# Performance work log

Hardware: AMD Instinct MI355X
Metric: run time of the kernel (lower is better)

Reference implementation:

```python
import jax, jax.numpy as jnp
import numpy as np

NEG = -9e15
EPS = 1e-5

# GraphAttention (classic GAT layer): h = xW; e_ij = LeakyReLU(a1.h_i + a2.h_j);
# attention = softmax(where(adj>0, e, -9e15)); out = attention @ h.
# The torch code builds one big block-diagonal adjacency; off-block entries get
# -9e15 and underflow to exactly 0 after softmax, so batched per-block GAT is
# numerically identical and avoids the O((B*N)^2) dense waste.

def gat(x, adj, W, a1, a2):
    h = jnp.einsum('bnf,fh->bnh', x, W)
    e = jax.nn.leaky_relu(jnp.einsum('bnh,h->bn', h, a1)[:, :, None]
                          + jnp.einsum('bnh,h->bn', h, a2)[:, None, :], 0.2)
    att = jax.nn.softmax(jnp.where(adj > 0, e, NEG), axis=-1)
    return jnp.einsum('bnm,bmh->bnh', att, h)

def mlp(x, W1, b1, W2, b2):
    return jax.nn.relu(x @ W1 + b1) @ W2 + b2


def setup_inputs() -> dict:
    key = jax.random.key(0)
    ks = iter(jax.random.split(key, 40))
    B, NV, NO = 8, 500, 1500
    DV, DO, H = 512, 32, 128

    def mat(din, dout):
        return jax.random.normal(next(ks), (din, dout), jnp.float32) / np.sqrt(din)

    def vec(d):
        return jax.random.normal(next(ks), (d,), jnp.float32) * 0.1

    inp = {
        'vis_memory': jax.random.normal(next(ks), (B, NV, DV), jnp.float32),
        'obj_memory': jax.random.normal(next(ks), (B, NO, DO), jnp.float32),
        'vis_adj': jax.random.uniform(next(ks), (B, NV, NV), jnp.float32),
        'obj_adj': jax.random.uniform(next(ks), (B, NO, NO), jnp.float32),
        'object_A_OV': jax.random.uniform(next(ks), (B, NO, NV), jnp.float32),
        # GAT layers
        'Wv1': mat(DV, H), 'av1a': vec(H), 'av1b': vec(H),
        'Wv2': mat(H, H),  'av2a': vec(H), 'av2b': vec(H),
        'Wo1': mat(DO, H), 'ao1a': vec(H), 'ao1b': vec(H),
        'Wo2': mat(H, H),  'ao2a': vec(H), 'ao2b': vec(H),
        # globalTobject / objectTglobal MLPs
        'g2o_W1': mat(H, H), 'g2o_b1': jnp.zeros((H,), jnp.float32),
        'g2o_W2': mat(H, H), 'g2o_b2': jnp.zeros((H,), jnp.float32),
        'o2g_W1': mat(H, H), 'o2g_b1': jnp.zeros((H,), jnp.float32),
        'o2g_W2': mat(H, H), 'o2g_b2': jnp.zeros((H,), jnp.float32),
        # output projections
        'img_W': mat(H, DV), 'img_b': jnp.zeros((DV,), jnp.float32),
        'obj_W': mat(H, DO), 'obj_b': jnp.zeros((DO,), jnp.float32),
    }
    return inp


def reference(vis_memory, obj_memory, vis_adj, obj_adj, object_A_OV,
              Wv1, av1a, av1b, Wv2, av2a, av2b,
              Wo1, ao1a, ao1b, Wo2, ao2a, ao2b,
              g2o_W1, g2o_b1, g2o_W2, g2o_b2,
              o2g_W1, o2g_b1, o2g_W2, o2g_b2,
              img_W, img_b, obj_W, obj_b):
    # cross adjacencies (block-diagonal in torch -> batched here)
    vo = jnp.swapaxes(object_A_OV, 1, 2)            # (B, NV, NO)
    vo = vo / (vo.sum(2, keepdims=True) + EPS)
    ov = jnp.swapaxes(vo, 1, 2)                     # (B, NO, NV)
    ov = ov / (ov.sum(2, keepdims=True) + EPS)

    v1 = jax.nn.relu(gat(vis_memory, vis_adj, Wv1, av1a, av1b))
    o1 = jax.nn.relu(gat(obj_memory, obj_adj, Wo1, ao1a, ao1b))
    vis = v1 + mlp(jnp.einsum('bvo,boh->bvh', vo, o1), o2g_W1, o2g_b1, o2g_W2, o2g_b2)
    obj = o1 + mlp(jnp.einsum('bov,bvh->boh', ov, v1), g2o_W1, g2o_b1, g2o_W2, g2o_b2)

    v2 = jax.nn.relu(gat(vis, vis_adj, Wv2, av2a, av2b))
    o2 = jax.nn.relu(gat(obj, obj_adj, Wo2, ao2a, ao2b))
    vis = v2 + mlp(jnp.einsum('bvo,boh->bvh', vo, o2), o2g_W1, o2g_b1, o2g_W2, o2g_b2)
    obj = o2 + mlp(jnp.einsum('bov,bvh->boh', ov, v2), g2o_W1, g2o_b1, g2o_W2, g2o_b2)

    vis_out = vis @ img_W + img_b                   # (B, NV, DV)
    obj_out = obj @ obj_W + obj_b                   # (B, NO, DO)
    return (vis_out, obj_out)
```

## Files before the change

### kernel.cpp

```cpp
#include <hip/hip_runtime.h>
#include <math.h>

#define EPSV 1e-5f
#define HD 128
#define IT 64
#define JT 32
#define WP 68
#define CCH 16
#define THR 256

typedef __attribute__((address_space(3))) uint32_t lds_u32_t;
typedef __attribute__((address_space(1))) uint32_t gbl_u32_t;
typedef __attribute__((ext_vector_type(8))) short bf16x8;
typedef __attribute__((ext_vector_type(4))) float f32x4;

__device__ __forceinline__ void async_copy16(const float* g, float* l) {
    __builtin_amdgcn_global_load_lds((const gbl_u32_t*)g, (lds_u32_t*)l, 16, 0, 0);
}

__device__ __forceinline__ void stage_tile_async(const float* gsrc, float* lds, int t) {
    int wv = t >> 6, lane = t & 63;
#pragma unroll
    for (int it = 0; it < 4; ++it) {
        int c = it * 4 + wv;
        async_copy16(gsrc + c * 256 + lane * 4, lds + c * 256);
    }
}

__device__ __forceinline__ void stage_8k(const void* g, void* l, int t) {
    const float* gf = (const float*)g; float* lf = (float*)l;
    async_copy16(gf + t * 4, lf + t * 4);
    async_copy16(gf + t * 4 + 1024, lf + t * 4 + 1024);
}

__device__ __forceinline__ unsigned int f2bf(float f) {
    return __builtin_bit_cast(unsigned int, f) >> 16;
}

__device__ __forceinline__ unsigned short rne_bf16(float f) {
    unsigned int u = __builtin_bit_cast(unsigned int, f);
    u += 0x7FFFu + ((u >> 16) & 1u);
    return (unsigned short)(u >> 16);
}

struct WprepP { const float *W, *a1, *a2; unsigned short* WT; float *wa1, *wa2; int K; };
struct XprepP { const float* X; unsigned short* Xbf; const float *wa1, *wa2;
                float *sa, *sb; int rows; };
struct GmfP   { const unsigned short *Xbf, *WT; unsigned short* hT; int N, tilesJ; };
struct AggP  { const float *adj, *sa, *sb, *sm; const unsigned short* hT;
               float *pp, *zp; int N, tiles, tilesJ, tps; };
struct CrossP{ const float *A, *src, *rs1; float *pp; int iN, jN, tiles, tps; };
struct FinP  { const float *pp, *zp; float *out; int rows, S; };
struct MlpP  { const float *pp, *scale; int S; const float *W1, *b1, *W2, *b2, *res;
               float *out; int rows; };


__global__ void colsum_part_k(const float* __restrict__ A, float* __restrict__ s1p,
                              int B, int NO, int NV) {
    int v = blockIdx.x * 256 + threadIdx.x;
    int c = blockIdx.y, b = blockIdx.z;
    if (v >= NV) return;
    int chunk = (NO + CCH - 1) / CCH;
    int o0 = c * chunk;
    int o1 = o0 + chunk; if (o1 > NO) o1 = NO;
    const float* Ab = A + (size_t)b * NO * NV + v;
    float s = 0.f;
    for (int o = o0; o < o1; ++o) s += Ab[(size_t)o * NV];
    s1p[((size_t)b * CCH + c) * NV + v] = s;
}

__global__ void colsum_fin_k(const float* __restrict__ s1p, float* __restrict__ rs1,
                             int B, int NV) {
    int idx = blockIdx.x * 256 + threadIdx.x;
    if (idx >= B * NV) return;
    int b = idx / NV, v = idx - b * NV;
    float s = 0.f;
    for (int c = 0; c < CCH; ++c) s += s1p[((size_t)b * CCH + c) * NV + v];
    rs1[idx] = 1.f / (s + EPSV);
}

__global__ void rowsum_inv_k(const float* __restrict__ A, const float* __restrict__ rs1,
                             float* __restrict__ rs2, int B, int NO, int NV) {
    int row = blockIdx.x * (blockDim.x >> 6) + (threadIdx.x >> 6);
    int lane = threadIdx.x & 63;
    if (row >= B * NO) return;
    int b = row / NO;
    const float* Ar = A + (size_t)row * NV;
    const float* r1 = rs1 + (size_t)b * NV;
    float s = 0.f;
    for (int v = lane; v < NV; v += 64) s += Ar[v] * r1[v];
    for (int off = 32; off; off >>= 1) s += __shfl_xor(s, off, 64);
    if (lane == 0) rs2[row] = 1.f / (s + EPSV);
}

__global__ __launch_bounds__(256)
void wprep_k(WprepP p0, WprepP p1, WprepP p2, WprepP p3, int e0, int e1, int e2) {
    __shared__ float lw[32][129];
    __shared__ float a1s[128], a2s[128];
    int bid = blockIdx.x;
    const WprepP& P = bid < e0 ? p0 : bid < e1 ? p1 : bid < e2 ? p2 : p3;
    int lb = bid < e0 ? bid : bid < e1 ? bid - e0 : bid < e2 ? bid - e1 : bid - e2;
    int k0 = lb * 32, K = P.K;
    int t = threadIdx.x;
    if (t < 128) { a1s[t] = P.a1[t]; a2s[t] = P.a2[t]; }
    for (int idx = t; idx < 32 * 32; idx += 256) {
        int kk = idx >> 5, c4 = idx & 31;
        float4 v = ((const float4*)(P.W + (size_t)(k0 + kk) * 128))[c4];
        lw[kk][c4 * 4 + 0] = v.x; lw[kk][c4 * 4 + 1] = v.y;
        lw[kk][c4 * 4 + 2] = v.z; lw[kk][c4 * 4 + 3] = v.w;
    }
    __syncthreads();
    int kk = t >> 3, g = t & 7;
    float s1 = 0.f, s2 = 0.f;
    for (int c = g; c < 128; c += 8) {
        float w = lw[kk][c];
        s1 = fmaf(w, a1s[c], s1);
        s2 = fmaf(w, a2s[c], s2);
    }
    s1 += __shfl_xor(s1, 1, 64); s1 += __shfl_xor(s1, 2, 64); s1 += __shfl_xor(s1, 4, 64);
    s2 += __shfl_xor(s2, 1, 64); s2 += __shfl_xor(s2, 2, 64); s2 += __shfl_xor(s2, 4, 64);
    if (g == 0) { P.wa1[k0 + kk] = s1; P.wa2[k0 + kk] = s2; }
    for (int idx = t; idx < 4096; idx += 256) {
        int c = idx >> 5, k = idx & 31;
        P.WT[(size_t)c * K + k0 + k] = rne_bf16(lw[k][c]);
    }
}

template<int K>
__device__ void xprep_body(const XprepP& P, int lb) {
    int t = threadIdx.x, wv = t >> 6, lane = t & 63;
    int row = lb * 4 + wv;
    if (row >= P.rows) return;
    const float4* x4 = (const float4*)(P.X + (size_t)row * K);
    const float4* w14 = (const float4*)P.wa1;
    const float4* w24 = (const float4*)P.wa2;
    unsigned short* xb = P.Xbf + (size_t)row * K;
    float s1 = 0.f, s2 = 0.f;
    constexpr int K4 = K / 4;
    constexpr int NI = (K4 + 63) / 64;
#pragma unroll
    for (int i = 0; i < NI; ++i) {
        int k4 = i * 64 + lane;
        if ((K4 % 64 == 0) || (k4 < K4)) {
            float4 x = x4[k4];
            float4 a = w14[k4];
            float4 b = w24[k4];
            s1 += x.x * a.x + x.y * a.y + x.z * a.z + x.w * a.w;
            s2 += x.x * b.x + x.y * b.y + x.z * b.z + x.w * b.w;
            ushort4 p = make_ushort4(rne_bf16(x.x), rne_bf16(x.y),
                                     rne_bf16(x.z), rne_bf16(x.w));
            *(ushort4*)(xb + (size_t)k4 * 4) = p;
        }
    }
#pragma unroll
    for (int off = 32; off; off >>= 1) {
        s1 += __shfl_xor(s1, off, 64);
        s2 += __shfl_xor(s2, off, 64);
    }
    if (lane == 0) { P.sa[row] = s1; P.sb[row] = s2; }
}

template<int KV, int KO>
__global__ __launch_bounds__(256)
void xprep2_k(XprepP V, XprepP O, int GV) {
    int bid = blockIdx.x;
    if (bid < GV) xprep_body<KV>(V, bid);
    else          xprep_body<KO>(O, bid - GV);
}

template<int K>
__device__ void gmf_body(const GmfP& P, int lb) {
    int tilesJ = P.tilesJ, N = P.N;
    int b = lb / tilesJ, jt = lb - b * tilesJ;
    int t = threadIdx.x, wv = t >> 6, lane = t & 63;
    int ml = lane & 15, quad = lane >> 4;
    const unsigned short* xb = P.Xbf + ((size_t)b * N + (size_t)jt * 32) * K;
    const unsigned short* wt0 = P.WT + (size_t)(wv * 32 + ml) * K;
    const unsigned short* wt1 = wt0 + (size_t)16 * K;
    const unsigned short* xb0 = xb + (size_t)ml * K;
    const unsigned short* xb1 = xb + (size_t)(16 + ml) * K;
    f32x4 acc00 = {0.f, 0.f, 0.f, 0.f}, acc01 = acc00, acc10 = acc00, acc11 = acc00;
#pragma unroll 4
    for (int kt = 0; kt < K / 32; ++kt) {
        int kk = kt * 32 + quad * 8;
        bf16x8 a0 = *(const bf16x8*)(wt0 + kk);
        bf16x8 a1 = *(const bf16x8*)(wt1 + kk);
        bf16x8 b0 = *(const bf16x8*)(xb0 + kk);
        bf16x8 b1 = *(const bf16x8*)(xb1 + kk);
        acc00 = __builtin_amdgcn_mfma_f32_16x16x32_bf16(a0, b0, acc00, 0, 0, 0);
        acc01 = __builtin_amdgcn_mfma_f32_16x16x32_bf16(a0, b1, acc01, 0, 0, 0);
        acc10 = __builtin_amdgcn_mfma_f32_16x16x32_bf16(a1, b0, acc10, 0, 0, 0);
        acc11 = __builtin_amdgcn_mfma_f32_16x16x32_bf16(a1, b1, acc11, 0, 0, 0);
    }
    unsigned short* hb = P.hT + (size_t)(b * tilesJ + jt) * 4096;
    int nvalid = N - jt * 32; if (nvalid > 32) nvalid = 32;
    bool ok0 = ml < nvalid, ok1 = (16 + ml) < nvalid;
    int c0 = wv * 32 + quad * 4;
#pragma unroll
    for (int r = 0; r < 4; ++r) {
        hb[(size_t)(c0 + r) * 32 + ml]           = ok0 ? rne_bf16(acc00[r]) : 0;
        hb[(size_t)(c0 + r) * 32 + 16 + ml]      = ok1 ? rne_bf16(acc01[r]) : 0;
        hb[(size_t)(c0 + 16 + r) * 32 + ml]      = ok0 ? rne_bf16(acc10[r]) : 0;
        hb[(size_t)(c0 + 16 + r) * 32 + 16 + ml] = ok1 ? rne_bf16(acc11[r]) : 0;
    }
}

template<int KV, int KO>
__global__ __launch_bounds__(256)
void gmf2_k(GmfP V, GmfP O, int GV) {
    int bid = blockIdx.x;
    if (bid < GV) gmf_body<KV>(V, bid);
    else          gmf_body<KO>(O, bid - GV);
}

__global__ __launch_bounds__(256)
void sbmax2_k(const float* __restrict__ sbV, float* __restrict__ smV,
              const float* __restrict__ sbO, float* __restrict__ smO,
              int NV, int NO) {
    __shared__ float red[256];
    int b0 = blockIdx.x, t = threadIdx.x;
    const float* sb; float* out; int N;
    if (b0 < 8) { sb = sbV + (size_t)b0 * NV; out = smV + b0; N = NV; }
    else        { sb = sbO + (size_t)(b0 - 8) * NO; out = smO + (b0 - 8); N = NO; }
    float m = -INFINITY;
    for (int j = t; j < N; j += 256) m = fmaxf(m, sb[j]);
    red[t] = m; __syncthreads();
    for (int s = 128; s; s >>= 1) {
        if (t < s) red[t] = fmaxf(red[t], red[t + s]);
        __syncthreads();
    }
    if (t == 0) *out = red[0];
}

struct SharedAggM {
    unsigned short hsT[2][128][32];
    unsigned short wsA[2][4][64][8];
    float sa_s[IT], m_s[IT];
};

__device__ void agg_body(SharedAggM& sm, const AggP& P, int lbid) {
    int tiles = P.tiles;
    int split = lbid / (8 * tiles);
    int rem = lbid - split * 8 * tiles;
    int b = rem / tiles;
    int i0 = (rem - b * tiles) * IT;
    int N = P.N;
    int jt0 = split * P.tps;
    if (jt0 >= P.tilesJ) return;
    int jt1 = jt0 + P.tps; if (jt1 > P.tilesJ) jt1 = P.tilesJ;
    int T = jt1 - jt0;
    int t = threadIdx.x;
    if (t < IT) {
        int i = i0 + t;
        float s = (i < N) ? P.sa[(size_t)b * N + i] : 0.f;
        sm.sa_s[t] = s;
        float e = s + P.sm[b];
        sm.m_s[t] = e > 0.f ? e : 0.2f * e;
    }
    __syncthreads();
    int wv = t >> 6, lane = t & 63;
    int il = t >> 2, j4 = (t & 3) * 4;
    int q0 = j4 >> 3, i0w = j4 & 7, wrow = il & 15;
    int nquad = lane >> 4, nlow = lane & 15;
    f32x4 acc[8];
#pragma unroll
    for (int nt = 0; nt < 8; ++nt)
#pragma unroll
        for (int r = 0; r < 4; ++r) acc[nt][r] = 0.f;
    float zacc = 0.f;
    const float* adjb = P.adj + ((size_t)b * N + i0) * N;
    const float* sbb = P.sb + (size_t)b * N;
    const unsigned short* hTb = P.hT + ((size_t)b * P.tilesJ + jt0) * 4096;
    int irow = i0 + il;
    stage_8k(hTb, &sm.hsT[0][0][0], t);
    float4 a4[2], s4[2];
#pragma unroll
    for (int k = 0; k < 2; ++k) {
        int j = jt0 * JT + j4 + k * 16;
        float4 av = make_float4(0.f,0.f,0.f,0.f), sv = make_float4(0.f,0.f,0.f,0.f);
        if (irow < N) {
            if (j + 3 < N) {
                av = *(const float4*)&adjb[(size_t)il * N + j];
                sv = *(const float4*)&sbb[j];
            } else {
                float* ap = (float*)&av; float* sp = (float*)&sv;
                for (int r = 0; r < 4; ++r)
                    if (j + r < N) { ap[r] = adjb[(size_t)il * N + j + r]; sp[r] = sbb[j + r]; }
            }
        }
        a4[k] = av; s4[k] = sv;
    }
    for (int tt = 0; tt < T; ++tt) {
        int cur = tt & 1;
        float sai = sm.sa_s[il], m = sm.m_s[il];
#pragma unroll
        for (int k = 0; k < 2; ++k) {
            float av[4] = {a4[k].x, a4[k].y, a4[k].z, a4[k].w};
            float sv[4] = {s4[k].x, s4[k].y, s4[k].z, s4[k].w};
            float w[4];
#pragma unroll
            for (int r = 0; r < 4; ++r) {
                float e = sai + sv[r];
                e = e > 0.f ? e : 0.2f * e;
                w[r] = av[r] > 0.f ? __expf(e - m) : 0.f;
                zacc += w[r];
            }
            unsigned int lo = f2bf(w[0]) | (__builtin_bit_cast(unsigned int, w[1]) & 0xFFFF0000u);
            unsigned int hi = f2bf(w[2]) | (__builtin_bit_cast(unsigned int, w[3]) & 0xFFFF0000u);
            uint2 pk = make_uint2(lo, hi);
            *(uint2*)&sm.wsA[cur][wv][wrow + 16 * (q0 + 2 * k)][i0w] = pk;
        }
        __syncthreads();
        if (tt + 1 < T) {
            stage_8k(hTb + (size_t)(tt + 1) * 4096, &sm.hsT[1 - cur][0][0], t);
#pragma unroll
            for (int k = 0; k < 2; ++k) {
                int j = (jt0 + tt + 1) * JT + j4 + k * 16;
                float4 av = make_float4(0.f,0.f,0.f,0.f), sv = make_float4(0.f,0.f,0.f,0.f);
                if (irow < N) {
                    if (j + 3 < N) {
                        av = *(const float4*)&adjb[(size_t)il * N + j];
                        sv = *(const float4*)&sbb[j];
                    } else {
                        float* ap = (float*)&av; float* sp = (float*)&sv;
                        for (int r = 0; r < 4; ++r)
                            if (j + r < N) { ap[r] = adjb[(size_t)il * N + j + r]; sp[r] = sbb[j + r]; }
                    }
                }
                a4[k] = av; s4[k] = sv;
            }
        }
        bf16x8 afrag = *(const bf16x8*)&sm.wsA[cur][wv][lane][0];
#pragma unroll
        for (int nt = 0; nt < 8; ++nt) {
            bf16x8 bfrag = *(const bf16x8*)&sm.hsT[cur][nt * 16 + nlow][nquad * 8];
            acc[nt] = __builtin_amdgcn_mfma_f32_16x16x32_bf16(afrag, bfrag, acc[nt], 0, 0, 0);
        }
    }
    zacc += __shfl_xor(zacc, 1, 64);
    zacc += __shfl_xor(zacc, 2, 64);
    size_t rowsTot = (size_t)8 * N;
    float* pp = P.pp + ((size_t)split * rowsTot + (size_t)b * N) * HD;
#pragma unroll
    for (int nt = 0; nt < 8; ++nt)
#pragma unroll
        for (int r = 0; r < 4; ++r) {
            int row = i0 + wv * 16 + nquad * 4 + r;
            if (row < N) pp[(size_t)row * HD + nt * 16 + nlow] = acc[nt][r];
        }
    if ((t & 3) == 0 && irow < N)
        P.zp[(size_t)split * rowsTot + (size_t)b * N + irow] = zacc;
}

__global__ __launch_bounds__(256)
void agg2_k(AggP V, AggP O, int GVb) {
    __shared__ SharedAggM sm;
    int bid = blockIdx.x;
    if (bid < GVb) agg_body(sm, V, bid);
    else           agg_body(sm, O, bid - GVb);
}

__device__ __forceinline__ void tile_fma256(const float (*hs)[HD], const float (*ws)[WP],
                                            int rg, int c0, float acc[4][8]) {
#pragma unroll 8
    for (int jl = 0; jl < JT; ++jl) {
        float4 h0 = *(const float4*)&hs[jl][c0];
        float4 h1 = *(const float4*)&hs[jl][c0 + 64];
        float4 w4 = *(const float4*)&ws[jl][rg * 4];
        float wq[4] = {w4.x, w4.y, w4.z, w4.w};
#pragma unroll
        for (int q = 0; q < 4; ++q) {
            float w = wq[q];
            acc[q][0] = fmaf(w, h0.x, acc[q][0]);
            acc[q][1] = fmaf(w, h0.y, acc[q][1]);
            acc[q][2] = fmaf(w, h0.z, acc[q][2]);
            acc[q][3] = fmaf(w, h0.w, acc[q][3]);
            acc[q][4] = fmaf(w, h1.x, acc[q][4]);
            acc[q][5] = fmaf(w, h1.y, acc[q][5]);
            acc[q][6] = fmaf(w, h1.z, acc[q][6]);
            acc[q][7] = fmaf(w, h1.w, acc[q][7]);
        }
    }
}

__device__ __forceinline__ void part_store256(float* __restrict__ pp, size_t base,
                                              int i0, int N, int rg, int c0,
                                              float acc[4][8]) {
#pragma unroll
    for (int q = 0; q < 4; ++q) {
        int i = i0 + rg * 4 + q;
        if (i >= N) continue;
        float* op = pp + base + (size_t)i * HD;
        *(float4*)&op[c0]      = make_float4(acc[q][0], acc[q][1], acc[q][2], acc[q][3]);
        *(float4*)&op[c0 + 64] = make_float4(acc[q][4], acc[q][5], acc[q][6], acc[q][7]);
    }
}

struct SharedTile { float hs[2][JT][HD]; float ws[2][JT][WP]; };

__device__ void cross_vo_body(SharedTile& sm, const CrossP& P, int lbid) {
    int tiles = P.tiles;
    int split = lbid / (8 * tiles);
    int rem = lbid - split * 8 * tiles;
    int b = rem / tiles;
    int i0 = (rem - b * tiles) * IT;
    int NVl = P.iN, NOl = P.jN;
    int j_begin = split * P.tps * JT;
    if (j_begin >= NOl) return;
    int j_end = j_begin + P.tps * JT;
    if (j_end > NOl) j_end = NOl;
    int T = (j_end - j_begin + JT - 1) / JT;
    int t = threadIdx.x;
    int rg = t >> 4, c0 = (t & 15) * 4;
    int il = t & 63, jlb = t >> 6;
    float acc[4][8];
#pragma unroll
    for (int q = 0; q < 4; ++q)
#pragma unroll
        for (int x = 0; x < 8; ++x) acc[q][x] = 0.f;
    const float* Ab = P.A + (size_t)b * NOl * NVl;
    const float* srcb = P.src + (size_t)b * NOl * HD;
    int v = i0 + il;
    float w8[8];
    stage_tile_async(srcb + (size_t)j_begin * HD, &sm.hs[0][0][0], t);
#pragma unroll
    for (int k = 0; k < 8; ++k) {
        int o = j_begin + jlb + k * 4;
        w8[k] = (v < NVl && o < NOl) ? Ab[(size_t)o * NVl + v] : 0.f;
    }
    for (int tt = 0; tt < T; ++tt) {
        int cur = tt & 1;
#pragma unroll
        for (int k = 0; k < 8; ++k) sm.ws[cur][jlb + k * 4][il] = w8[k];
        __syncthreads();
        if (tt + 1 < T) {
            int jn = j_begin + (tt + 1) * JT;
            stage_tile_async(srcb + (size_t)jn * HD, &sm.hs[1 - cur][0][0], t);
#pragma unroll
            for (int k = 0; k < 8; ++k) {
                int o = jn + jlb + k * 4;
                w8[k] = (v < NVl && o < NOl) ? Ab[(size_t)o * NVl + v] : 0.f;
            }
        }
        tile_fma256(sm.hs[cur], sm.ws[cur], rg, c0, acc);
    }
    size_t rowsTot = (size_t)8 * NVl;
    part_store256(P.pp, ((size_t)split * rowsTot + (size_t)b * NVl) * HD, i0, NVl, rg, c0, acc);
}

__device__ void cross_ov_body(SharedTile& sm, const CrossP& P, int lbid) {
    int tiles = P.tiles;
    int split = lbid / (8 * tiles);
    int rem = lbid - split * 8 * tiles;
    int b = rem / tiles;
    int i0 = (rem - b * tiles) * IT;
    int NOl = P.iN, NVl = P.jN;
    int j_begin = split * P.tps * JT;
    if (j_begin >= NVl) return;
    int j_end = j_begin + P.tps * JT;
    if (j_end > NVl) j_end = NVl;
    int T = (j_end - j_begin + JT - 1) / JT;
    int t = threadIdx.x;
    int rg = t >> 4, c0 = (t & 15) * 4;
    int il = t >> 2, j4 = (t & 3) * 4;
    float acc[4][8];
#pragma unroll
    for (int q = 0; q < 4; ++q)
#pragma unroll
        for (int x = 0; x < 8; ++x) acc[q][x] = 0.f;
    const float* Ab = P.A + (size_t)b * NOl * NVl;
    const float* srcb = P.src + (size_t)b * NVl * HD;
    const float* r1b = P.rs1 + (size_t)b * NVl;
    int orow = i0 + il;
    float4 a4[2], r4[2];
    stage_tile_async(srcb + (size_t)j_begin * HD, &sm.hs[0][0][0], t);
#pragma unroll
    for (int k = 0; k < 2; ++k) {
        int vv = j_begin + j4 + k * 16;
        float4 av = make_float4(0.f,0.f,0.f,0.f), rv = make_float4(0.f,0.f,0.f,0.f);
        if (orow < NOl) {
            if (vv + 3 < NVl) {
                av = *(const float4*)&Ab[(size_t)orow * NVl + vv];
                rv = *(const float4*)&r1b[vv];
            } else {
                float* ap = (float*)&av; float* rp = (float*)&rv;
                for (int r = 0; r < 4; ++r)
                    if (vv + r < NVl) { ap[r] = Ab[(size_t)orow * NVl + vv + r]; rp[r] = r1b[vv + r]; }
            }
        }
        a4[k] = av; r4[k] = rv;
    }
    for (int tt = 0; tt < T; ++tt) {
        int cur = tt & 1;
#pragma unroll
        for (int k = 0; k < 2; ++k) {
            float wv[4] = {a4[k].x * r4[k].x, a4[k].y * r4[k].y,
                           a4[k].z * r4[k].z, a4[k].w * r4[k].w};
#pragma unroll
            for (int r = 0; r < 4; ++r) sm.ws[cur][j4 + r + k * 16][il] = wv[r];
        }
        __syncthreads();
        if (tt + 1 < T) {
            int jn = j_begin + (tt + 1) * JT;
            stage_tile_async(srcb + (size_t)jn * HD, &sm.hs[1 - cur][0][0], t);
#pragma unroll
            for (int k = 0; k < 2; ++k) {
                int vv = jn + j4 + k * 16;
                float4 av = make_float4(0.f,0.f,0.f,0.f), rv = make_float4(0.f,0.f,0.f,0.f);
                if (orow < NOl) {
                    if (vv + 3 < NVl) {
                        av = *(const float4*)&Ab[(size_t)orow * NVl + vv];
                        rv = *(const float4*)&r1b[vv];
                    } else {
                        float* ap = (float*)&av; float* rp = (float*)&rv;
                        for (int r = 0; r < 4; ++r)
                            if (vv + r < NVl) { ap[r] = Ab[(size_t)orow * NVl + vv + r]; rp[r] = r1b[vv + r]; }
                    }
                }
                a4[k] = av; r4[k] = rv;
            }
        }
        tile_fma256(sm.hs[cur], sm.ws[cur], rg, c0, acc);
    }
    size_t rowsTot = (size_t)8 * NOl;
    part_store256(P.pp, ((size_t)split * rowsTot + (size_t)b * NOl) * HD, i0, NOl, rg, c0, acc);
}

__global__ __launch_bounds__(256)
void cross2_k(CrossP VO, CrossP OV, int GVOb) {
    __shared__ SharedTile sm;
    int bid = blockIdx.x;
    if (bid < GVOb) cross_vo_body(sm, VO, bid);
    else            cross_ov_body(sm, OV, bid - GVOb);
}

__global__ __launch_bounds__(256)
void fin2_k(FinP V, FinP O, int GVb) {
    int bid = blockIdx.x;
    const FinP& P = (bid < GVb) ? V : O;
    int idx = ((bid < GVb) ? bid : bid - GVb) * 256 + threadIdx.x;
    int rows = P.rows;
    int row = idx >> 5;
    if (row >= rows) return;
    float4 v = make_float4(0.f, 0.f, 0.f, 0.f);
    for (int s = 0; s < P.S; ++s) {
        float4 p = ((const float4*)P.pp)[((size_t)s * rows + row) * 32 + (idx & 31)];
        v.x += p.x; v.y += p.y; v.z += p.z; v.w += p.w;
    }
    float z = 0.f;
    for (int s = 0; s < P.S; ++s) z += P.zp[(size_t)s * rows + row];
    float sc = 1.f / z;
    v.x = fmaxf(v.x * sc, 0.f); v.y = fmaxf(v.y * sc, 0.f);
    v.z = fmaxf(v.z * sc, 0.f); v.w = fmaxf(v.w * sc, 0.f);
    ((float4*)P.out)[idx] = v;
}

__global__ __launch_bounds__(128)
void mlp2_k(MlpP V, MlpP O, int GVb) {
    __shared__ float xs[8][HD];
    __shared__ float hh[8][HD];
    int bid = blockIdx.x;
    const MlpP& P = (bid < GVb) ? V : O;
    int row0 = ((bid < GVb) ? bid : bid - GVb) * 8;
    int rows = P.rows;
    int t = threadIdx.x;
    for (int l = t; l < 8 * 32; l += 128) {
        int r = l >> 5, c4 = l & 31;
        int row = row0 + r;
        float4 v = make_float4(0.f, 0.f, 0.f, 0.f);
        if (row < rows) {
            for (int s = 0; s < P.S; ++s) {
                float4 p = ((const float4*)P.pp)[((size_t)s * rows + row) * 32 + c4];
                v.x += p.x; v.y += p.y; v.z += p.z; v.w += p.w;
            }
            float sc = P.scale[row];
            v.x *= sc; v.y *= sc; v.z *= sc; v.w *= sc;
        }
        ((float4*)&xs[r][0])[c4] = v;
    }
    __syncthreads();
    int wv = t >> 6, tt = t & 63, rb = wv * 4;
    float a0[4] = {0.f, 0.f, 0.f, 0.f}, a1v[4] = {0.f, 0.f, 0.f, 0.f};
#pragma unroll 4
    for (int k = 0; k < HD; ++k) {
        float w0 = P.W1[(size_t)k * HD + tt];
        float w1 = P.W1[(size_t)k * HD + tt + 64];
#pragma unroll
        for (int r = 0; r < 4; ++r) {
            float x = xs[rb + r][k];
            a0[r] = fmaf(x, w0, a0[r]);
            a1v[r] = fmaf(x, w1, a1v[r]);
        }
    }
    float bb0 = P.b1[tt], bb1 = P.b1[tt + 64];
#pragma unroll
    for (int r = 0; r < 4; ++r) {
        hh[rb + r][tt]      = fmaxf(a0[r] + bb0, 0.f);
        hh[rb + r][tt + 64] = fmaxf(a1v[r] + bb1, 0.f);
    }
    __syncthreads();
    float c0a[4] = {0.f, 0.f, 0.f, 0.f}, c1a[4] = {0.f, 0.f, 0.f, 0.f};
#pragma unroll 4
    for (int k = 0; k < HD; ++k) {
        float w0 = P.W2[(size_t)k * HD + tt];
        float w1 = P.W2[(size_t)k * HD + tt + 64];
#pragma unroll
        for (int r = 0; r < 4; ++r) {
            float x = hh[rb + r][k];
            c0a[r] = fmaf(x, w0, c0a[r]);
            c1a[r] = fmaf(x, w1, c1a[r]);
        }
    }
    float d0 = P.b2[tt], d1 = P.b2[tt + 64];
#pragma unroll
    for (int r = 0; r < 4; ++r) {
        int row = row0 + rb + r;
        if (row >= rows) continue;
        P.out[(size_t)row * HD + tt]      = c0a[r] + d0 + P.res[(size_t)row * HD + tt];
        P.out[(size_t)row * HD + tt + 64] = c1a[r] + d1 + P.res[(size_t)row * HD + tt + 64];
    }
}

template<int RELU, int BIAS, int RES>
__global__ __launch_bounds__(128)
void linear_k(const float* __restrict__ X, const float* __restrict__ W,
              const float* __restrict__ bias, const float* __restrict__ res,
              float* __restrict__ out, int rows, int K, int Dout) {
    __shared__ float xs[4][512];
    int row0 = blockIdx.x * 4;
    int t = threadIdx.x;
    int K4 = K >> 2;
    for (int l = t; l < 4 * K4; l += 128) {
        int r = l / K4, c4 = l - r * K4;
        float4 val = make_float4(0.f, 0.f, 0.f, 0.f);
        if (row0 + r < rows) val = ((const float4*)(X + (size_t)(row0 + r) * K))[c4];
        ((float4*)&xs[r][0])[c4] = val;
    }
    __syncthreads();
    int chunk = Dout < 256 ? Dout : 256;
    int half = chunk >> 1;
    if (t >= half) return;
    int c0 = blockIdx.y * chunk + t;
    int c1 = c0 + half;
    float a00 = 0, a01 = 0, a02 = 0, a03 = 0, a10 = 0, a11 = 0, a12 = 0, a13 = 0;
#pragma unroll 4
    for (int k = 0; k < K; ++k) {
        float w0 = W[(size_t)k * Dout + c0];
        float w1 = W[(size_t)k * Dout + c1];
        float x0 = xs[0][k], x1 = xs[1][k], x2 = xs[2][k], x3 = xs[3][k];
        a00 = fmaf(x0, w0, a00); a01 = fmaf(x1, w0, a01);
        a02 = fmaf(x2, w0, a02); a03 = fmaf(x3, w0, a03);
        a10 = fmaf(x0, w1, a10); a11 = fmaf(x1, w1, a11);
        a12 = fmaf(x2, w1, a12); a13 = fmaf(x3, w1, a13);
    }
    float accs[2][4] = {{a00, a01, a02, a03}, {a10, a11, a12, a13}};
    int cs[2] = {c0, c1};
    for (int h = 0; h < 2; ++h) {
        float bv = BIAS ? bias[cs[h]] : 0.f;
        for (int r = 0; r < 4; ++r) {
            int row = row0 + r;
            if (row >= rows) continue;
            float v = accs[h][r] + bv;
            if (RES) v += res[(size_t)row * Dout + cs[h]];
            if (RELU) v = fmaxf(v, 0.f);
            out[(size_t)row * Dout + cs[h]] = v;
        }
    }
}

extern "C" void kernel_launch(void* const* d_in, const int* in_sizes, int n_in,
                              void* d_out, int out_size, void* d_ws, size_t ws_size,
                              hipStream_t stream) {
    const int B = 8, NV = 500, NO = 1500, DV = 512, DO = 32;
    const float* vis_memory = (const float*)d_in[0];
    const float* obj_memory = (const float*)d_in[1];
    const float* vis_adj    = (const float*)d_in[2];
    const float* obj_adj    = (const float*)d_in[3];
    const float* A_OV       = (const float*)d_in[4];
    const float* Wv1  = (const float*)d_in[5];
    const float* av1a = (const float*)d_in[6];
    const float* av1b = (const float*)d_in[7];
    const float* Wv2  = (const float*)d_in[8];
    const float* av2a = (const float*)d_in[9];
    const float* av2b = (const float*)d_in[10];
    const float* Wo1  = (const float*)d_in[11];
    const float* ao1a = (const float*)d_in[12];
    const float* ao1b = (const float*)d_in[13];
    const float* Wo2  = (const float*)d_in[14];
    const float* ao2a = (const float*)d_in[15];
    const float* ao2b = (const float*)d_in[16];
    const float* g2o_W1 = (const float*)d_in[17];
    const float* g2o_b1 = (const float*)d_in[18];
    const float* g2o_W2 = (const float*)d_in[19];
    const float* g2o_b2 = (const float*)d_in[20];
    const float* o2g_W1 = (const float*)d_in[21];
    const float* o2g_b1 = (const float*)d_in[22];
    const float* o2g_W2 = (const float*)d_in[23];
    const float* o2g_b2 = (const float*)d_in[24];
    const float* img_W = (const float*)d_in[25];
    const float* img_b = (const float*)d_in[26];
    const float* obj_W = (const float*)d_in[27];
    const float* obj_b = (const float*)d_in[28];

    const int tilesJV = 16, tilesJO = 47;

    float* wsp = (float*)d_ws;
    size_t off = 0;
    auto alloc = [&](size_t n) { float* p = wsp + off; off += (n + 3) & ~(size_t)3; return p; };
    float* rs1   = alloc(B * NV);
    float* rs2   = alloc(B * NO);
    float* saV   = alloc(B * NV);
    float* sbV   = alloc(B * NV);
    float* smV   = alloc(B);
    float* saO   = alloc(B * NO);
    float* sbO   = alloc(B * NO);
    float* smO   = alloc(B);
    float* s1p   = alloc((size_t)B * CCH * NV);
    unsigned short* WTv1 = (unsigned short*)alloc(128 * 512 / 2);
    unsigned short* WTo1 = (unsigned short*)alloc(128 * 32 / 2);
    unsigned short* WTv2 = (unsigned short*)alloc(128 * 128 / 2);
    unsigned short* WTo2 = (unsigned short*)alloc(128 * 128 / 2);
    float* wav1a = alloc(512); float* wav1b = alloc(512);
    float* wao1a = alloc(32);  float* wao1b = alloc(32);
    float* wav2a = alloc(128); float* wav2b = alloc(128);
    float* wao2a = alloc(128); float* wao2b = alloc(128);
    unsigned short* XbfV = (unsigned short*)alloc((size_t)B * NV * 512 / 2);
    unsigned short* XbfO = (unsigned short*)alloc((size_t)B * NO * 128 / 2);
    unsigned short* hTv = (unsigned short*)alloc((size_t)B * tilesJV * 4096 / 2);
    unsigned short* hTo = (unsigned short*)alloc((size_t)B * tilesJO * 4096 / 2);
    float* v1    = alloc((size_t)B * NV * HD);
    float* o1    = alloc((size_t)B * NO * HD);
    float* visb  = alloc((size_t)B * NV * HD);
    float* objb  = alloc((size_t)B * NO * HD);
    float* ppV   = alloc((size_t)8 * B * NV * HD);
    float* zpV   = alloc((size_t)8 * B * NV);
    float* ppO   = alloc((size_t)4 * B * NO * HD);
    float* zpO   = alloc((size_t)4 * B * NO);
    alloc(16384);

    {
        WprepP w0{Wv1, av1a, av1b, WTv1, wav1a, wav1b, DV};
        WprepP w1{Wo1, ao1a, ao1b, WTo1, wao1a, wao1b, DO};
        WprepP w2{Wv2, av2a, av2b, WTv2, wav2a, wav2b, HD};
        WprepP w3{Wo2, ao2a, ao2b, WTo2, wao2a, wao2b, HD};
        wprep_k<<<25, 256, 0, stream>>>(w0, w1, w2, w3, 16, 17, 21);
    }

    colsum_part_k<<<dim3((NV + 255) / 256, CCH, B), 256, 0, stream>>>(A_OV, s1p, B, NO, NV);
    colsum_fin_k<<<dim3((B * NV + 255) / 256), 256, 0, stream>>>(s1p, rs1, B, NV);
    rowsum_inv_k<<<dim3((B * NO + 3) / 4), 256, 0, stream>>>(A_OV, rs1, rs2, B, NO, NV);

    const int tilesV = 8, tilesO = 24;
    const int SV = 8, SO = 4, SVO = 8, SOV = 4;
    const int tpsV = 2;
    const int tpsO = 12;
    const int tpsVO = 6;
    const int tpsOV = 4;
    const int G_AGG_V = B * tilesV * SV;
    const int G_AGG_O = B * tilesO * SO;
    const int G_CR_VO = B * tilesV * SVO;
    const int G_CR_OV = B * tilesO * SOV;
    const int G_MLP_V = B * NV / 8;
    const int G_MLP_O = B * NO / 8;
    const int G_FIN_V = B * NV * 32 / 256;
    const int G_FIN_O = B * NO * 32 / 256;
    const int G_XP_V = B * NV / 4;
    const int G_XP_O = B * NO / 4;
    const int G_GMF_V = B * tilesJV;
    const int G_GMF_O = B * tilesJO;

    auto tail = [&](float* visout, float* objout) {
        sbmax2_k<<<16, 256, 0, stream>>>(sbV, smV, sbO, smO, NV, NO);
        AggP av{vis_adj, saV, sbV, smV, hTv, ppV, zpV, NV, tilesV, tilesJV, tpsV};
        AggP ao{obj_adj, saO, sbO, smO, hTo, ppO, zpO, NO, tilesO, tilesJO, tpsO};
        agg2_k<<<G_AGG_V + G_AGG_O, THR, 0, stream>>>(av, ao, G_AGG_V);
        FinP fv{ppV, zpV, v1, B * NV, SV};
        FinP fo{ppO, zpO, o1, B * NO, SO};
        fin2_k<<<G_FIN_V + G_FIN_O, 256, 0, stream>>>(fv, fo, G_FIN_V);
        CrossP cvo{A_OV, o1, nullptr, ppV, NV, NO, tilesV, tpsVO};
        CrossP cov{A_OV, v1, rs1, ppO, NO, NV, tilesO, tpsOV};
        cross2_k<<<G_CR_VO + G_CR_OV, THR, 0, stream>>>(cvo, cov, G_CR_VO);
        MlpP mv{ppV, rs1, SVO, o2g_W1, o2g_b1, o2g_W2, o2g_b2, v1, visout, B * NV};
        MlpP mo{ppO, rs2, SOV, g2o_W1, g2o_b1, g2o_W2, g2o_b2, o1, objout, B * NO};
        mlp2_k<<<G_MLP_V + G_MLP_O, 128, 0, stream>>>(mv, mo, G_MLP_V);
    };

    {
        XprepP xv{vis_memory, XbfV, wav1a, wav1b, saV, sbV, B * NV};
        XprepP xo{obj_memory, XbfO, wao1a, wao1b, saO, sbO, B * NO};
        xprep2_k<512, 32><<<G_XP_V + G_XP_O, 256, 0, stream>>>(xv, xo, G_XP_V);
        GmfP gv{XbfV, WTv1, hTv, NV, tilesJV};
        GmfP go{XbfO, WTo1, hTo, NO, tilesJO};
        gmf2_k<512, 32><<<G_GMF_V + G_GMF_O, 256, 0, stream>>>(gv, go, G_GMF_V);
        tail(visb, objb);
    }
    {
        XprepP xv{visb, XbfV, wav2a, wav2b, saV, sbV, B * NV};
        XprepP xo{objb, XbfO, wao2a, wao2b, saO, sbO, B * NO};
        xprep2_k<128, 128><<<G_XP_V + G_XP_O, 256, 0, stream>>>(xv, xo, G_XP_V);
        GmfP gv{XbfV, WTv2, hTv, NV, tilesJV};
        GmfP go{XbfO, WTo2, hTo, NO, tilesJO};
        gmf2_k<128, 128><<<G_GMF_V + G_GMF_O, 256, 0, stream>>>(gv, go, G_GMF_V);
        tail(visb, objb);
    }

    float* vis_out = (float*)d_out;
    float* obj_out = vis_out + (size_t)B * NV * DV;
    linear_k<0, 1, 0><<<dim3((B * NV + 3) / 4, (DV + 255) / 256), 128, 0, stream>>>(
        visb, img_W, img_b, nullptr, vis_out, B * NV, HD, DV);
    linear_k<0, 1, 0><<<dim3((B * NO + 3) / 4, 1), 128, 0, stream>>>(
        objb, obj_W, obj_b, nullptr, obj_out, B * NO, HD, DO);
}
```

Before: 615.0 us.

## Deepen adjacency prefetch to two tiles with manual waitcnt and unrolled double buffer

```diff
diff --git a/kernel.cpp b/kernel.cpp
--- a/kernel.cpp
+++ b/kernel.cpp
@@ -238,6 +238,57 @@
     float sa_s[IT], m_s[IT];
 };
 
+__device__ __forceinline__ void load_adj(const float* adjb, const float* sbb,
+                                         int il, int j4, int irow, int N,
+                                         int jt, float4* AR, float4* SR) {
+#pragma unroll
+    for (int k = 0; k < 2; ++k) {
+        int j = jt * JT + j4 + k * 16;
+        bool okc = (j + 3) < N;
+        bool ok = (irow < N) && okc;
+        size_t offa = ok ? (size_t)il * N + j : 0;
+        int offs = okc ? j : 0;
+        float4 av = *(const float4*)(adjb + offa);
+        float4 sv = *(const float4*)(sbb + offs);
+        float msk = ok ? 1.f : 0.f;
+        av.x *= msk; av.y *= msk; av.z *= msk; av.w *= msk;
+        AR[k] = av; SR[k] = sv;
+    }
+}
+
+#define AGG_TILE(tt_, CUR_, AR_, SR_) do {                                          \
+    float sai_ = sm.sa_s[il], mm_ = sm.m_s[il];                                     \
+    _Pragma("unroll")                                                               \
+    for (int k = 0; k < 2; ++k) {                                                   \
+        float av_[4] = {AR_[k].x, AR_[k].y, AR_[k].z, AR_[k].w};                    \
+        float sv_[4] = {SR_[k].x, SR_[k].y, SR_[k].z, SR_[k].w};                    \
+        float w_[4];                                                                \
+        _Pragma("unroll")                                                           \
+        for (int r = 0; r < 4; ++r) {                                               \
+            float e_ = sai_ + sv_[r];                                               \
+            e_ = e_ > 0.f ? e_ : 0.2f * e_;                                         \
+            w_[r] = av_[r] > 0.f ? __expf(e_ - mm_) : 0.f;                          \
+            zacc += w_[r];                                                          \
+        }                                                                           \
+        unsigned int lo_ = f2bf(w_[0]) | (__builtin_bit_cast(unsigned int, w_[1]) & 0xFFFF0000u); \
+        unsigned int hi_ = f2bf(w_[2]) | (__builtin_bit_cast(unsigned int, w_[3]) & 0xFFFF0000u); \
+        *(uint2*)&sm.wsA[CUR_][wv][wrow + 16 * (q0 + 2 * k)][i0w] = make_uint2(lo_, hi_); \
+    }                                                                               \
+       \
+    if (tt_ + 1 < T) asm volatile("s_waitcnt vmcnt(4) lgkmcnt(0)" ::: "memory");    \
+    else             asm volatile("s_waitcnt vmcnt(0) lgkmcnt(0)" ::: "memory");    \
+    __builtin_amdgcn_s_barrier();                                                   \
+    asm volatile("" ::: "memory");      \
+    if (tt_ + 1 < T) stage_8k(hTb + (size_t)(tt_ + 1) * 4096, &sm.hsT[1 - CUR_][0][0], t); \
+    if (tt_ + 2 < T) load_adj(adjb, sbb, il, j4, irow, N, jt0 + tt_ + 2, AR_, SR_); \
+    bf16x8 afrag_ = *(const bf16x8*)&sm.wsA[CUR_][wv][lane][0];                     \
+    _Pragma("unroll")                                                               \
+    for (int nt = 0; nt < 8; ++nt) {                                                \
+        bf16x8 bfrag_ = *(const bf16x8*)&sm.hsT[CUR_][nt * 16 + nlow][nquad * 8];   \
+        acc[nt] = __builtin_amdgcn_mfma_f32_16x16x32_bf16(afrag_, bfrag_, acc[nt], 0, 0, 0); \
+    }                                                                               \
+} while (0)
+
 __device__ void agg_body(SharedAggM& sm, const AggP& P, int lbid) {
     int tiles = P.tiles;
     int split = lbid / (8 * tiles);
@@ -272,70 +323,16 @@
     const float* sbb = P.sb + (size_t)b * N;
     const unsigned short* hTb = P.hT + ((size_t)b * P.tilesJ + jt0) * 4096;
     int irow = i0 + il;
+    float4 aA[2], sA[2], aB[2], sB[2];
     stage_8k(hTb, &sm.hsT[0][0][0], t);
-    float4 a4[2], s4[2];
-#pragma unroll
-    for (int k = 0; k < 2; ++k) {
-        int j = jt0 * JT + j4 + k * 16;
-        float4 av = make_float4(0.f,0.f,0.f,0.f), sv = make_float4(0.f,0.f,0.f,0.f);
-        if (irow < N) {
-            if (j + 3 < N) {
-                av = *(const float4*)&adjb[(size_t)il * N + j];
-                sv = *(const float4*)&sbb[j];
-            } else {
-                float* ap = (float*)&av; float* sp = (float*)&sv;
-                for (int r = 0; r < 4; ++r)
-                    if (j + r < N) { ap[r] = adjb[(size_t)il * N + j + r]; sp[r] = sbb[j + r]; }
-            }
-        }
-        a4[k] = av; s4[k] = sv;
-    }
-    for (int tt = 0; tt < T; ++tt) {
-        int cur = tt & 1;
-        float sai = sm.sa_s[il], m = sm.m_s[il];
-#pragma unroll
-        for (int k = 0; k < 2; ++k) {
-            float av[4] = {a4[k].x, a4[k].y, a4[k].z, a4[k].w};
-            float sv[4] = {s4[k].x, s4[k].y, s4[k].z, s4[k].w};
-            float w[4];
-#pragma unroll
-            for (int r = 0; r < 4; ++r) {
-                float e = sai + sv[r];
-                e = e > 0.f ? e : 0.2f * e;
-                w[r] = av[r] > 0.f ? __expf(e - m) : 0.f;
-                zacc += w[r];
-            }
-            unsigned int lo = f2bf(w[0]) | (__builtin_bit_cast(unsigned int, w[1]) & 0xFFFF0000u);
-            unsigned int hi = f2bf(w[2]) | (__builtin_bit_cast(unsigned int, w[3]) & 0xFFFF0000u);
-            uint2 pk = make_uint2(lo, hi);
-            *(uint2*)&sm.wsA[cur][wv][wrow + 16 * (q0 + 2 * k)][i0w] = pk;
-        }
-        __syncthreads();
-        if (tt + 1 < T) {
-            stage_8k(hTb + (size_t)(tt + 1) * 4096, &sm.hsT[1 - cur][0][0], t);
-#pragma unroll
-            for (int k = 0; k < 2; ++k) {
-                int j = (jt0 + tt + 1) * JT + j4 + k * 16;
-                float4 av = make_float4(0.f,0.f,0.f,0.f), sv = make_float4(0.f,0.f,0.f,0.f);
-                if (irow < N) {
-                    if (j + 3 < N) {
-                        av = *(const float4*)&adjb[(size_t)il * N + j];
-                        sv = *(const float4*)&sbb[j];
-                    } else {
-                        float* ap = (float*)&av; float* sp = (float*)&sv;
-                        for (int r = 0; r < 4; ++r)
-                            if (j + r < N) { ap[r] = adjb[(size_t)il * N + j + r]; sp[r] = sbb[j + r]; }
-                    }
-                }
-                a4[k] = av; s4[k] = sv;
-            }
-        }
-        bf16x8 afrag = *(const bf16x8*)&sm.wsA[cur][wv][lane][0];
-#pragma unroll
-        for (int nt = 0; nt < 8; ++nt) {
-            bf16x8 bfrag = *(const bf16x8*)&sm.hsT[cur][nt * 16 + nlow][nquad * 8];
-            acc[nt] = __builtin_amdgcn_mfma_f32_16x16x32_bf16(afrag, bfrag, acc[nt], 0, 0, 0);
-        }
+    load_adj(adjb, sbb, il, j4, irow, N, jt0, aA, sA);
+    if (1 < T) load_adj(adjb, sbb, il, j4, irow, N, jt0 + 1, aB, sB);
+    int tt = 0;
+    while (true) {
+        AGG_TILE(tt, 0, aA, sA);
+        ++tt; if (tt >= T) break;
+        AGG_TILE(tt, 1, aB, sB);
+        ++tt; if (tt >= T) break;
     }
     zacc += __shfl_xor(zacc, 1, 64);
     zacc += __shfl_xor(zacc, 2, 64);
```

After: 601.2 us. 2.2% less time.

## Precompute adjacency bitmasks once, swizzle hT layout, triple-buffer agg staging

Applied to the files above, without the earlier changes.

```diff
diff --git a/kernel.cpp b/kernel.cpp
--- a/kernel.cpp
+++ b/kernel.cpp
@@ -47,7 +47,8 @@
 struct XprepP { const float* X; unsigned short* Xbf; const float *wa1, *wa2;
                 float *sa, *sb; int rows; };
 struct GmfP   { const unsigned short *Xbf, *WT; unsigned short* hT; int N, tilesJ; };
-struct AggP  { const float *adj, *sa, *sb, *sm; const unsigned short* hT;
+struct MaskP  { const float* adj; unsigned int* maskT; int N, tilesJ, chunks; };
+struct AggP  { const unsigned int* mask; const float *sa, *sb, *sm; const unsigned short* hT;
                float *pp, *zp; int N, tiles, tilesJ, tps; };
 struct CrossP{ const float *A, *src, *rs1; float *pp; int iN, jN, tiles, tps; };
 struct FinP  { const float *pp, *zp; float *out; int rows, S; };
@@ -91,6 +92,27 @@
     for (int v = lane; v < NV; v += 64) s += Ar[v] * r1[v];
     for (int off = 32; off; off >>= 1) s += __shfl_xor(s, off, 64);
     if (lane == 0) rs2[row] = 1.f / (s + EPSV);
+}
+
+__global__ __launch_bounds__(256)
+void mask2_k(MaskP V, MaskP O, int GV) {
+    int bid = blockIdx.x;
+    const MaskP& P = (bid < GV) ? V : O;
+    int lb = (bid < GV) ? bid : bid - GV;
+    int t = threadIdx.x;
+    int wid = lb * 4 + (t >> 6), lane = t & 63;
+    int N = P.N, chunks = P.chunks, tilesJ = P.tilesJ;
+    int row = wid / chunks;
+    int ch = wid - row * chunks;
+    if (row >= 8 * N) return;
+    int b = row / N, i = row - b * N;
+    int j = ch * 64 + lane;
+    float v = (j < N) ? P.adj[(size_t)row * N + j] : 0.f;
+    unsigned long long m = __ballot(v > 0.f);
+    size_t base = (size_t)b * tilesJ * N;
+    int w0 = ch * 2;
+    if (lane == 0)                      P.maskT[base + (size_t)w0 * N + i] = (unsigned int)m;
+    if (lane == 32 && w0 + 1 < tilesJ)  P.maskT[base + (size_t)(w0 + 1) * N + i] = (unsigned int)(m >> 32);
 }
 
 __global__ __launch_bounds__(256)
@@ -198,10 +220,12 @@
     int c0 = wv * 32 + quad * 4;
 #pragma unroll
     for (int r = 0; r < 4; ++r) {
-        hb[(size_t)(c0 + r) * 32 + ml]           = ok0 ? rne_bf16(acc00[r]) : 0;
-        hb[(size_t)(c0 + r) * 32 + 16 + ml]      = ok1 ? rne_bf16(acc01[r]) : 0;
-        hb[(size_t)(c0 + 16 + r) * 32 + ml]      = ok0 ? rne_bf16(acc10[r]) : 0;
-        hb[(size_t)(c0 + 16 + r) * 32 + 16 + ml] = ok1 ? rne_bf16(acc11[r]) : 0;
+        int ca = c0 + r, cb = c0 + 16 + r;
+        int swa = ((ca >> 1) & 3) << 3, swb = ((cb >> 1) & 3) << 3;
+        hb[ca * 32 + (ml ^ swa)]        = ok0 ? rne_bf16(acc00[r]) : 0;
+        hb[ca * 32 + ((16 + ml) ^ swa)] = ok1 ? rne_bf16(acc01[r]) : 0;
+        hb[cb * 32 + (ml ^ swb)]        = ok0 ? rne_bf16(acc10[r]) : 0;
+        hb[cb * 32 + ((16 + ml) ^ swb)] = ok1 ? rne_bf16(acc11[r]) : 0;
     }
 }
 
@@ -233,8 +257,10 @@
 }
 
 struct SharedAggM {
-    unsigned short hsT[2][128][32];
+    unsigned short hsT[3][128][32];
     unsigned short wsA[2][4][64][8];
+    unsigned int mask_s[12][64];
+    float sb_s[12 * 32];
     float sa_s[IT], m_s[IT];
 };
 
@@ -257,83 +283,71 @@
         float e = s + P.sm[b];
         sm.m_s[t] = e > 0.f ? e : 0.2f * e;
     }
+    for (int idx = t; idx < (T << 6); idx += 256) {
+        int w = idx >> 6, r = idx & 63;
+        int ir = i0 + r;
+        sm.mask_s[w][r] = (ir < N)
+            ? P.mask[((size_t)b * P.tilesJ + jt0 + w) * N + ir] : 0u;
+    }
+    const float* sbb = P.sb + (size_t)b * N;
+    for (int idx = t; idx < (T << 5); idx += 256) {
+        int j = (jt0 << 5) + idx;
+        sm.sb_s[idx] = (j < N) ? sbb[j] : 0.f;
+    }
     __syncthreads();
+    const unsigned short* hTb = P.hT + ((size_t)b * P.tilesJ + jt0) * 4096;
+    stage_8k(hTb, &sm.hsT[0][0][0], t);
+    if (T > 1) stage_8k(hTb + 4096, &sm.hsT[1][0][0], t);
+
     int wv = t >> 6, lane = t & 63;
     int il = t >> 2, j4 = (t & 3) * 4;
     int q0 = j4 >> 3, i0w = j4 & 7, wrow = il & 15;
     int nquad = lane >> 4, nlow = lane & 15;
+    int nq2 = (nquad ^ ((nlow >> 1) & 3)) * 8;
     f32x4 acc[8];
 #pragma unroll
     for (int nt = 0; nt < 8; ++nt)
 #pragma unroll
         for (int r = 0; r < 4; ++r) acc[nt][r] = 0.f;
     float zacc = 0.f;
-    const float* adjb = P.adj + ((size_t)b * N + i0) * N;
-    const float* sbb = P.sb + (size_t)b * N;
-    const unsigned short* hTb = P.hT + ((size_t)b * P.tilesJ + jt0) * 4096;
     int irow = i0 + il;
-    stage_8k(hTb, &sm.hsT[0][0][0], t);
-    float4 a4[2], s4[2];
-#pragma unroll
-    for (int k = 0; k < 2; ++k) {
-        int j = jt0 * JT + j4 + k * 16;
-        float4 av = make_float4(0.f,0.f,0.f,0.f), sv = make_float4(0.f,0.f,0.f,0.f);
-        if (irow < N) {
-            if (j + 3 < N) {
-                av = *(const float4*)&adjb[(size_t)il * N + j];
-                sv = *(const float4*)&sbb[j];
-            } else {
-                float* ap = (float*)&av; float* sp = (float*)&sv;
-                for (int r = 0; r < 4; ++r)
-                    if (j + r < N) { ap[r] = adjb[(size_t)il * N + j + r]; sp[r] = sbb[j + r]; }
-            }
-        }
-        a4[k] = av; s4[k] = sv;
-    }
+    const float4* sb4 = (const float4*)sm.sb_s;
     for (int tt = 0; tt < T; ++tt) {
-        int cur = tt & 1;
+        int cur = tt - (tt / 3) * 3;
+        unsigned int mw = sm.mask_s[tt][il];
+        float4 sA = sb4[tt * 8 + (t & 3)];
+        float4 sB = sb4[tt * 8 + (t & 3) + 4];
         float sai = sm.sa_s[il], m = sm.m_s[il];
 #pragma unroll
         for (int k = 0; k < 2; ++k) {
-            float av[4] = {a4[k].x, a4[k].y, a4[k].z, a4[k].w};
-            float sv[4] = {s4[k].x, s4[k].y, s4[k].z, s4[k].w};
-            float w[4];
+            float sv[4];
+            { float4 s4 = k ? sB : sA; sv[0] = s4.x; sv[1] = s4.y; sv[2] = s4.z; sv[3] = s4.w; }
+            float w_[4];
 #pragma unroll
             for (int r = 0; r < 4; ++r) {
                 float e = sai + sv[r];
                 e = e > 0.f ? e : 0.2f * e;
-                w[r] = av[r] > 0.f ? __expf(e - m) : 0.f;
-                zacc += w[r];
+                float ww = __expf(e - m);
+                ww = ((mw >> (j4 + k * 16 + r)) & 1u) ? ww : 0.f;
+                zacc += ww;
+                w_[r] = ww;
             }
-            unsigned int lo = f2bf(w[0]) | (__builtin_bit_cast(unsigned int, w[1]) & 0xFFFF0000u);
-            unsigned int hi = f2bf(w[2]) | (__builtin_bit_cast(unsigned int, w[3]) & 0xFFFF0000u);
-            uint2 pk = make_uint2(lo, hi);
-            *(uint2*)&sm.wsA[cur][wv][wrow + 16 * (q0 + 2 * k)][i0w] = pk;
-        }
-        __syncthreads();
-        if (tt + 1 < T) {
-            stage_8k(hTb + (size_t)(tt + 1) * 4096, &sm.hsT[1 - cur][0][0], t);
-#pragma unroll
-            for (int k = 0; k < 2; ++k) {
-                int j = (jt0 + tt + 1) * JT + j4 + k * 16;
-                float4 av = make_float4(0.f,0.f,0.f,0.f), sv = make_float4(0.f,0.f,0.f,0.f);
-                if (irow < N) {
-                    if (j + 3 < N) {
-                        av = *(const float4*)&adjb[(size_t)il * N + j];
-                        sv = *(const float4*)&sbb[j];
-                    } else {
-                        float* ap = (float*)&av; float* sp = (float*)&sv;
-                        for (int r = 0; r < 4; ++r)
-                            if (j + r < N) { ap[r] = adjb[(size_t)il * N + j + r]; sp[r] = sbb[j + r]; }
-                    }
-                }
-                a4[k] = av; s4[k] = sv;
-            }
-        }
-        bf16x8 afrag = *(const bf16x8*)&sm.wsA[cur][wv][lane][0];
+            unsigned int lo = f2bf(w_[0]) | (__builtin_bit_cast(unsigned int, w_[1]) & 0xFFFF0000u);
+            unsigned int hi = f2bf(w_[2]) | (__builtin_bit_cast(unsigned int, w_[3]) & 0xFFFF0000u);
+            *(uint2*)&sm.wsA[tt & 1][wv][wrow + 16 * (q0 + 2 * k)][i0w] = make_uint2(lo, hi);
+        }
+        if (tt + 1 < T) asm volatile("s_waitcnt vmcnt(2) lgkmcnt(0)" ::: "memory");
+        else            asm volatile("s_waitcnt vmcnt(0) lgkmcnt(0)" ::: "memory");
+        __builtin_amdgcn_s_barrier();
+        asm volatile("" ::: "memory");
+        if (tt + 2 < T) {
+            int nb = tt + 2; nb -= (nb / 3) * 3;
+            stage_8k(hTb + (size_t)(tt + 2) * 4096, &sm.hsT[nb][0][0], t);
+        }
+        bf16x8 afrag = *(const bf16x8*)&sm.wsA[tt & 1][wv][lane][0];
 #pragma unroll
         for (int nt = 0; nt < 8; ++nt) {
-            bf16x8 bfrag = *(const bf16x8*)&sm.hsT[cur][nt * 16 + nlow][nquad * 8];
+            bf16x8 bfrag = *(const bf16x8*)&sm.hsT[cur][nt * 16 + nlow][nq2];
             acc[nt] = __builtin_amdgcn_mfma_f32_16x16x32_bf16(afrag, bfrag, acc[nt], 0, 0, 0);
         }
     }
@@ -716,6 +730,8 @@
     float* sbO   = alloc(B * NO);
     float* smO   = alloc(B);
     float* s1p   = alloc((size_t)B * CCH * NV);
+    unsigned int* maskV = (unsigned int*)alloc((size_t)B * tilesJV * NV);
+    unsigned int* maskO = (unsigned int*)alloc((size_t)B * tilesJO * NO);
     unsigned short* WTv1 = (unsigned short*)alloc(128 * 512 / 2);
     unsigned short* WTo1 = (unsigned short*)alloc(128 * 32 / 2);
     unsigned short* WTv2 = (unsigned short*)alloc(128 * 128 / 2);
@@ -745,6 +761,15 @@
         WprepP w3{Wo2, ao2a, ao2b, WTo2, wao2a, wao2b, HD};
         wprep_k<<<25, 256, 0, stream>>>(w0, w1, w2, w3, 16, 17, 21);
     }
+    {
+        const int chunksV = (NV + 63) / 64;
+        const int chunksO = (NO + 63) / 64;
+        const int G_MSK_V = B * NV * chunksV / 4;
+        const int G_MSK_O = B * NO * chunksO / 4;
+        MaskP mv{vis_adj, maskV, NV, tilesJV, chunksV};
+        MaskP mo{obj_adj, maskO, NO, tilesJO, chunksO};
+        mask2_k<<<G_MSK_V + G_MSK_O, 256, 0, stream>>>(mv, mo, G_MSK_V);
+    }
 
     colsum_part_k<<<dim3((NV + 255) / 256, CCH, B), 256, 0, stream>>>(A_OV, s1p, B, NO, NV);
     colsum_fin_k<<<dim3((B * NV + 255) / 256), 256, 0, stream>>>(s1p, rs1, B, NV);
@@ -771,8 +796,8 @@
 
     auto tail = [&](float* visout, float* objout) {
         sbmax2_k<<<16, 256, 0, stream>>>(sbV, smV, sbO, smO, NV, NO);
-        AggP av{vis_adj, saV, sbV, smV, hTv, ppV, zpV, NV, tilesV, tilesJV, tpsV};
-        AggP ao{obj_adj, saO, sbO, smO, hTo, ppO, zpO, NO, tilesO, tilesJO, tpsO};
+        AggP av{maskV, saV, sbV, smV, hTv, ppV, zpV, NV, tilesV, tilesJV, tpsV};
+        AggP ao{maskO, saO, sbO, smO, hTo, ppO, zpO, NO, tilesO, tilesJO, tpsO};
         agg2_k<<<G_AGG_V + G_AGG_O, THR, 0, stream>>>(av, ao, G_AGG_V);
         FinP fv{ppV, zpV, v1, B * NV, SV};
         FinP fo{ppO, zpO, o1, B * NO, SO};
```

New measurement: 623.3 us. No clear change (+1.3%).
